# Performance work log

Measured on AMD Instinct MI355X. Metric: run time of the kernel, lower is better.

## Reference

```python
import jax, jax.numpy as jnp
import numpy as np

B, P, C = 4, 2048, 1024
N_HEADS = 16
HEAD = C // N_HEADS


def setup_inputs() -> dict:
    key = jax.random.key(0)
    ks = jax.random.split(key, 9)
    s = C ** -0.5
    return {
        "x": jax.random.normal(ks[0], (B, P, C), dtype=jnp.float32),
        "Wq": jax.random.normal(ks[1], (C, C), dtype=jnp.float32) * s,
        "bq": jnp.zeros((C,), dtype=jnp.float32),
        "Wk": jax.random.normal(ks[2], (C, C), dtype=jnp.float32) * s,
        "bk": jnp.zeros((C,), dtype=jnp.float32),
        "Wv": jax.random.normal(ks[3], (C, C), dtype=jnp.float32) * s,
        "bv": jnp.zeros((C,), dtype=jnp.float32),
        "Wo": jax.random.normal(ks[4], (C, C), dtype=jnp.float32) * s,
        "bo": jnp.zeros((C,), dtype=jnp.float32),
    }


def _attn(x, Wq, bq, Wk, bk, Wv, bv, Wo, bo):
    b, p, c = x.shape
    q = (x @ Wq + bq).reshape(b, p, N_HEADS, HEAD).transpose(0, 2, 1, 3)
    k = (x @ Wk + bk).reshape(b, p, N_HEADS, HEAD).transpose(0, 2, 1, 3)
    v = (x @ Wv + bv).reshape(b, p, N_HEADS, HEAD).transpose(0, 2, 1, 3)
    # scores: [B, H, P, P]
    w = jnp.einsum('bhqd,bhkd->bhqk', q, k) * (HEAD ** -0.5)
    w = jax.nn.softmax(w, axis=-1)
    y = jnp.einsum('bhqk,bhkd->bhqd', w, v)
    y = y.transpose(0, 2, 1, 3).reshape(b, p, c)
    return y @ Wo + bo


def reference(x, Wq, bq, Wk, bk, Wv, bv, Wo, bo):
    return _attn(x, Wq, bq, Wk, bk, Wv, bv, Wo, bo)
```

## Files before the change

kernel.cpp:

```cpp
#include <hip/hip_runtime.h>

#define B_DIM 4
#define P_DIM 2048
#define C_DIM 1024
#define H_CNT 16
#define D_HEAD 64
#define M_DIM 8192
#define K_DIM 1024

typedef __attribute__((ext_vector_type(4))) float  f32x4;
typedef __attribute__((ext_vector_type(8))) __bf16 bf16x8;
typedef __attribute__((ext_vector_type(4))) __bf16 bf16x4;
typedef __attribute__((ext_vector_type(4))) short  s16x4;
typedef __attribute__((ext_vector_type(8))) short  s16x8;

static __device__ __forceinline__ short f2bf(float f) {
    unsigned u = __float_as_uint(f);
    u += 0x7fff + ((u >> 16) & 1);
    return (short)(u >> 16);
}

#define GLDS16(src, dst) __builtin_amdgcn_global_load_lds( \
    (__attribute__((address_space(1))) void*)(void*)(src), \
    (__attribute__((address_space(3))) void*)(void*)(dst), 16, 0, 0)

__global__ __launch_bounds__(256) void cvt_f32_bf16(const float* __restrict__ in,
                                                    short* __restrict__ out) {
    size_t i = ((size_t)blockIdx.x * 256 + threadIdx.x) * 4;
    f32x4 v = *(const f32x4*)(in + i);
    s16x4 o;
    o[0] = f2bf(v[0]); o[1] = f2bf(v[1]); o[2] = f2bf(v[2]); o[3] = f2bf(v[3]);
    *(s16x4*)(out + i) = o;
}

__global__ __launch_bounds__(256) void wtrans_all(const float* __restrict__ W0,
                                                  const float* __restrict__ W1,
                                                  const float* __restrict__ W2,
                                                  const float* __restrict__ W3,
                                                  short* __restrict__ WT) {
    __shared__ float t[32][33];
    const int z = blockIdx.z;
    const float* W = z == 0 ? W0 : z == 1 ? W1 : z == 2 ? W2 : W3;
    short* dst = WT + (size_t)z * C_DIM * C_DIM;
    const int k0 = blockIdx.y * 32, n0 = blockIdx.x * 32;
    const int tx = threadIdx.x & 31, ty = threadIdx.x >> 5;
#pragma unroll
    for (int j = 0; j < 4; ++j)
        t[ty + j * 8][tx] = W[(size_t)(k0 + ty + j * 8) * C_DIM + n0 + tx];
    __syncthreads();
#pragma unroll
    for (int j = 0; j < 4; ++j)
        dst[(size_t)(n0 + ty + j * 8) * C_DIM + k0 + tx] = f2bf(t[tx][ty + j * 8]);
}

__global__ __launch_bounds__(512, 2) void gemm_qk8(const short* __restrict__ A,
                                                   const short* __restrict__ BT,
                                                   const float* __restrict__ bias,
                                                   const float* __restrict__ bias2,
                                                   short* __restrict__ outp) {
    __shared__ __align__(16) short lA[2][256 * 64];
    __shared__ __align__(16) short lB[2][256 * 64];
    const int tid = threadIdx.x;
    const int lane = tid & 63;
    const int w = tid >> 6;
    const int wm = w >> 2, wn = w & 3;
    const int li = lane & 15, g = lane >> 4;

    const int flat = blockIdx.y * 8 + blockIdx.x;
    const int lid = (flat & 7) * 32 + (flat >> 3);
    const int m0 = (lid >> 3) * 256;
    const int n0 = (lid & 7) * 256;

    const int e0 = tid, e1 = tid + 512;
    const int r0 = e0 >> 3, lu0 = (e0 & 7) ^ (r0 & 7);
    const int r1 = e1 >> 3, lu1 = (e1 & 7) ^ (r1 & 7);
    const short* aS0 = A + (size_t)(m0 + r0) * K_DIM + lu0 * 8;
    const short* aS1 = A + (size_t)(m0 + r1) * K_DIM + lu1 * 8;
    const short* bS0 = BT + (size_t)(n0 + r0) * K_DIM + lu0 * 8;
    const short* bS1 = BT + (size_t)(n0 + r1) * K_DIM + lu1 * 8;
    const int dA0 = e0 * 8, dA1 = e1 * 8;

#define STAGE_A8(buf, hh, kt) do { \
    GLDS16(aS0 + (size_t)(hh) * 128 * K_DIM + (kt) * 64, &lA[buf][(hh) * 8192 + dA0]); \
    GLDS16(aS1 + (size_t)(hh) * 128 * K_DIM + (kt) * 64, &lA[buf][(hh) * 8192 + dA1]); } while (0)
#define STAGE_B8(buf, hh, kt) do { \
    GLDS16(bS0 + (size_t)(hh) * 128 * K_DIM + (kt) * 64, &lB[buf][(hh) * 8192 + dB0]); \
    GLDS16(bS1 + (size_t)(hh) * 128 * K_DIM + (kt) * 64, &lB[buf][(hh) * 8192 + dB1]); } while (0)
    const int dB0 = dA0, dB1 = dA1;

    int aoff[8][2], boff[4][2];
#pragma unroll
    for (int mrep = 0; mrep < 8; ++mrep) {
        const int row = wm * 128 + mrep * 16 + li;
#pragma unroll
        for (int ks = 0; ks < 2; ++ks)
            aoff[mrep][ks] = row * 64 + (((ks * 4 + g) ^ (row & 7)) * 8);
    }
#pragma unroll
    for (int nrep = 0; nrep < 4; ++nrep) {
        const int row = wn * 64 + nrep * 16 + li;
#pragma unroll
        for (int ks = 0; ks < 2; ++ks)
            boff[nrep][ks] = row * 64 + (((ks * 4 + g) ^ (row & 7)) * 8);
    }

    f32x4 acc[8][4] = {};

    STAGE_A8(0, 0, 0); STAGE_A8(0, 1, 0);
    STAGE_B8(0, 0, 0); STAGE_B8(0, 1, 0);
    asm volatile("s_waitcnt vmcnt(0)" ::: "memory");
    __builtin_amdgcn_s_barrier();

    for (int t = 0; t < 16; ++t) {
        const int buf = t & 1;
        const short* LA = lA[buf];
        const short* LB = lB[buf];
        bf16x8 bf[4][2];
#pragma unroll
        for (int p = 0; p < 4; ++p) {
            if (p == 0) {
#pragma unroll
                for (int nrep = 0; nrep < 4; ++nrep)
#pragma unroll
                    for (int ks = 0; ks < 2; ++ks)
                        bf[nrep][ks] = *(const bf16x8*)&LB[boff[nrep][ks]];
            }
            bf16x8 af2[2][2];
#pragma unroll
            for (int i = 0; i < 2; ++i)
#pragma unroll
                for (int ks = 0; ks < 2; ++ks)
                    af2[i][ks] = *(const bf16x8*)&LA[aoff[2 * p + i][ks]];
            if (t < 15) {
                if (p == 0)      STAGE_A8(buf ^ 1, 0, t + 1);
                else if (p == 1) STAGE_A8(buf ^ 1, 1, t + 1);
                else if (p == 2) STAGE_B8(buf ^ 1, 0, t + 1);
                else             STAGE_B8(buf ^ 1, 1, t + 1);
            }
            __builtin_amdgcn_s_barrier();
            __builtin_amdgcn_s_setprio(1);
#pragma unroll
            for (int ks = 0; ks < 2; ++ks)
#pragma unroll
                for (int i = 0; i < 2; ++i)
#pragma unroll
                    for (int j = 0; j < 4; ++j)
                        acc[2 * p + i][j] = __builtin_amdgcn_mfma_f32_16x16x32_bf16(
                            bf[j][ks], af2[i][ks], acc[2 * p + i][j], 0, 0, 0);
            __builtin_amdgcn_s_setprio(0);
            __builtin_amdgcn_s_barrier();
        }
        asm volatile("s_waitcnt vmcnt(0)" ::: "memory");
        __builtin_amdgcn_s_barrier();
    }

#pragma unroll
    for (int nrep = 0; nrep < 4; ++nrep) {
        const int nb = n0 + wn * 64 + nrep * 16 + 4 * g;
        const float* bp = nb < 1024 ? bias : bias2;
        const float sc = nb < 1024 ? 0.125f : 1.0f;
        const f32x4 bb = *(const f32x4*)&bp[nb & 1023];
        const int hI = (nb >> 6) & 15, d = nb & 63;
        short* base = outp + (size_t)(nb >> 10) * M_DIM * C_DIM;
#pragma unroll
        for (int mrep = 0; mrep < 8; ++mrep) {
            const int m = m0 + wm * 128 + mrep * 16 + li;
            const int bI = m >> 11, p = m & 2047;
            s16x4 v4;
#pragma unroll
            for (int r = 0; r < 4; ++r) v4[r] = f2bf((acc[mrep][nrep][r] + bb[r]) * sc);
            *(s16x4*)&base[(((size_t)bI * H_CNT + hI) * P_DIM + p) * D_HEAD + d] = v4;
        }
    }
#undef STAGE_A8
#undef STAGE_B8
}

template<int MODE>
__global__ __launch_bounds__(256) void gemm_bt(const short* __restrict__ A,
                                               const short* __restrict__ BT,
                                               const float* __restrict__ bias,
                                               const float* __restrict__ bias2,
                                               void* __restrict__ outp,
                                               int gx) {
    const int h = blockIdx.y * gx + blockIdx.x;
    const int cpx = (gx << 6) >> 3;
    const int lid = (h & 7) * cpx + (h >> 3);
    const int m0 = (lid / gx) * 128;
    const int n0 = (lid % gx) * 128;

    __shared__ __align__(16) short lA[128 * 32];
    __shared__ __align__(16) short lB[128 * 32];
    const int tid = threadIdx.x;
    const int lane = tid & 63;
    const int w = tid >> 6;
    const int wr = (w >> 1) * 64;
    const int wc = (w & 1) * 64;
    const int li = lane & 15, g = lane >> 4;

    f32x4 acc[4][4] = {};

    const int r0s = tid >> 2, r1s = (tid + 256) >> 2;
    const int c0 = (tid & 3) ^ ((r0s >> 1) & 3);
    const int c1 = (tid & 3) ^ ((r1s >> 1) & 3);
    const short* a0 = A + (size_t)(m0 + r0s) * K_DIM + c0 * 8;
    const short* a1 = A + (size_t)(m0 + r1s) * K_DIM + c1 * 8;
    const short* b0 = BT + (size_t)(n0 + r0s) * K_DIM + c0 * 8;
    const short* b1 = BT + (size_t)(n0 + r1s) * K_DIM + c1 * 8;
    short* lA0 = lA + w * 512;  short* lA1 = lA + 2048 + w * 512;
    short* lB0 = lB + w * 512;  short* lB1 = lB + 2048 + w * 512;

    int aoff[4], boff[4];
#pragma unroll
    for (int i = 0; i < 4; ++i) {
        int ra = wr + i * 16 + li;  int pa = g ^ ((ra >> 1) & 3);
        aoff[i] = ra * 32 + pa * 8;
        int rb = wc + i * 16 + li;  int pb = g ^ ((rb >> 1) & 3);
        boff[i] = rb * 32 + pb * 8;
    }

    for (int k0 = 0; k0 < K_DIM; k0 += 32) {
        __syncthreads();
        GLDS16(a0 + k0, lA0);
        GLDS16(a1 + k0, lA1);
        GLDS16(b0 + k0, lB0);
        GLDS16(b1 + k0, lB1);
        __syncthreads();
        bf16x8 af[4], bfr[4];
#pragma unroll
        for (int i = 0; i < 4; ++i) {
            af[i]  = *(const bf16x8*)&lA[aoff[i]];
            bfr[i] = *(const bf16x8*)&lB[boff[i]];
        }
#pragma unroll
        for (int i = 0; i < 4; ++i)
#pragma unroll
            for (int j = 0; j < 4; ++j) {
                if (MODE == 2)
                    acc[i][j] = __builtin_amdgcn_mfma_f32_16x16x32_bf16(
                        af[i], bfr[j], acc[i][j], 0, 0, 0);
                else
                    acc[i][j] = __builtin_amdgcn_mfma_f32_16x16x32_bf16(
                        bfr[j], af[i], acc[i][j], 0, 0, 0);
            }
    }

    if (MODE == 1) {
#pragma unroll
        for (int j = 0; j < 4; ++j) {
            const int nb = n0 + wc + j * 16 + 4 * g;
            const f32x4 bb = *(const f32x4*)&bias[nb];
#pragma unroll
            for (int i = 0; i < 4; ++i) {
                const int m = m0 + wr + i * 16 + li;
                f32x4 v;
#pragma unroll
                for (int r = 0; r < 4; ++r) v[r] = acc[i][j][r] + bb[r];
                *(f32x4*)&((float*)outp)[(size_t)m * C_DIM + nb] = v;
            }
        }
    } else {
#pragma unroll
        for (int j = 0; j < 4; ++j) {
            const int nn = n0 + wc + j * 16 + li;
            const float bb = bias[nn];
            const int hI = nn >> 6, d = nn & 63;
#pragma unroll
            for (int i = 0; i < 4; ++i) {
                const int pbse = m0 + wr + i * 16 + 4 * g;
                const int bI = pbse >> 11, p = pbse & 2047;
                s16x4 v4;
#pragma unroll
                for (int r = 0; r < 4; ++r) v4[r] = f2bf(acc[i][j][r] + bb);
                *(s16x4*)&((short*)outp)[(((size_t)bI * H_CNT + hI) * D_HEAD + d) * P_DIM + p] = v4;
            }
        }
    }
}

__global__ __launch_bounds__(256, 4) void attn_fwd(const short* __restrict__ Q,
                                                   const short* __restrict__ Kb,
                                                   const short* __restrict__ VT,
                                                   short* __restrict__ Y) {
    const int flat = blockIdx.y * 16 + blockIdx.x;
    const int xcd = flat & 7, rr = flat >> 3;
    const int bh = xcd + 8 * (rr >> 4);
    const int qx = rr & 15;

    const int b = bh >> 4, h = bh & 15;
    const int tid = threadIdx.x;
    const int w = tid >> 6, lane = tid & 63;
    const int li = lane & 15, g = lane >> 4;
    const int x7 = li & 7;
    const int q0 = qx * 128 + w * 32;
    const short* Qh = Q + (size_t)bh * P_DIM * D_HEAD;
    const short* Kh = Kb + (size_t)bh * P_DIM * D_HEAD;
    const short* Vh = VT + (size_t)bh * D_HEAD * P_DIM;

    __shared__ __align__(16) short lK[64 * 64];
    __shared__ __align__(16) short lV[64 * 64];
    __shared__ __align__(16) short pb[4][32 * 64];
    short* pw = pb[w];

    bf16x8 qf[2][2];
#pragma unroll
    for (int qt = 0; qt < 2; ++qt)
#pragma unroll
        for (int c = 0; c < 2; ++c)
            qf[qt][c] = *(const bf16x8*)&Qh[(size_t)(q0 + qt * 16 + li) * D_HEAD + c * 32 + g * 8];

    f32x4 o[2][4] = {};
    float ps[2] = {};

    const int t1 = tid + 256;
    const int r0 = tid >> 3, u0 = (tid & 7) ^ (r0 & 7);
    const int r1 = t1 >> 3,  u1 = (t1 & 7) ^ (r1 & 7);
    const short* ks0 = Kh + r0 * D_HEAD + u0 * 8;
    const short* ks1 = Kh + r1 * D_HEAD + u1 * 8;
    const short* vs0 = Vh + r0 * P_DIM + u0 * 8;
    const short* vs1 = Vh + r1 * P_DIM + u1 * 8;
    short* dk0 = lK + tid * 8;  short* dk1 = lK + t1 * 8;
    short* dv0 = lV + tid * 8;  short* dv1 = lV + t1 * 8;

    const int pwrow0 = li * 64;
    const int wsw = x7 << 1;

    for (int k0 = 0; k0 < P_DIM; k0 += 64) {
        __syncthreads();
        GLDS16(ks0 + (size_t)k0 * D_HEAD, dk0);
        GLDS16(ks1 + (size_t)k0 * D_HEAD, dk1);
        GLDS16(vs0 + k0, dv0);
        GLDS16(vs1 + k0, dv1);
        __syncthreads();

        bf16x8 kf[4][2];
#pragma unroll
        for (int kt = 0; kt < 4; ++kt) {
            const int rbase = (kt * 16 + li) * 64;
            kf[kt][0] = *(const bf16x8*)&lK[rbase + ((0 + g) ^ x7) * 8];
            kf[kt][1] = *(const bf16x8*)&lK[rbase + ((4 + g) ^ x7) * 8];
        }

#pragma unroll
        for (int qt = 0; qt < 2; ++qt) {
            f32x4 s[4] = {};
#pragma unroll
            for (int kt = 0; kt < 4; ++kt) {
                s[kt] = __builtin_amdgcn_mfma_f32_16x16x32_bf16(kf[kt][0], qf[qt][0], s[kt], 0, 0, 0);
                s[kt] = __builtin_amdgcn_mfma_f32_16x16x32_bf16(kf[kt][1], qf[qt][1], s[kt], 0, 0, 0);
            }
            const int rowb = pwrow0 + qt * 16 * 64;
#pragma unroll
            for (int kt = 0; kt < 4; ++kt) {
                bf16x4 pv4;
#pragma unroll
                for (int r = 0; r < 4; ++r) {
                    float e = __expf(s[kt][r]);
                    ps[qt] += e;
                    pv4[r] = (__bf16)e;
                }
                const int j = (kt * 4 + g) ^ wsw;
                *(bf16x4*)&pw[rowb + j * 4] = pv4;
            }
        }
        __builtin_amdgcn_sched_barrier(0);
        asm volatile("s_waitcnt lgkmcnt(0)" ::: "memory");
        __builtin_amdgcn_sched_barrier(0);
#pragma unroll
        for (int kc = 0; kc < 2; ++kc) {
            bf16x8 pf[2];
#pragma unroll
            for (int qt = 0; qt < 2; ++qt) {
                const int j = (8 * kc + 2 * g) ^ wsw;
                pf[qt] = *(const bf16x8*)&pw[(qt * 16 + li) * 64 + j * 4];
            }
#pragma unroll
            for (int dt = 0; dt < 4; ++dt) {
                bf16x8 vf = *(const bf16x8*)&lV[(dt * 16 + li) * 64 + ((kc * 4 + g) ^ x7) * 8];
                o[0][dt] = __builtin_amdgcn_mfma_f32_16x16x32_bf16(pf[0], vf, o[0][dt], 0, 0, 0);
                o[1][dt] = __builtin_amdgcn_mfma_f32_16x16x32_bf16(pf[1], vf, o[1][dt], 0, 0, 0);
            }
        }
    }

#pragma unroll
    for (int qt = 0; qt < 2; ++qt) {
        float v = ps[qt];
        v += __shfl_xor(v, 16);
        v += __shfl_xor(v, 32);
#pragma unroll
        for (int r = 0; r < 4; ++r) {
            const float inv = 1.0f / __shfl(v, 4 * g + r);
            const int p = q0 + qt * 16 + 4 * g + r;
            short* yrow = Y + ((size_t)b * P_DIM + p) * C_DIM + h * D_HEAD;
#pragma unroll
            for (int dt = 0; dt < 4; ++dt)
                yrow[dt * 16 + li] = f2bf(o[qt][dt][r] * inv);
        }
    }
}

extern "C" void kernel_launch(void* const* d_in, const int* in_sizes, int n_in,
                              void* d_out, int out_size, void* d_ws, size_t ws_size,
                              hipStream_t stream) {
    (void)in_sizes; (void)n_in; (void)out_size; (void)ws_size;
    const float* x  = (const float*)d_in[0];
    const float* Wq = (const float*)d_in[1];
    const float* bq = (const float*)d_in[2];
    const float* Wk = (const float*)d_in[3];
    const float* bk = (const float*)d_in[4];
    const float* Wv = (const float*)d_in[5];
    const float* bv = (const float*)d_in[6];
    const float* Wo = (const float*)d_in[7];
    const float* bo = (const float*)d_in[8];

    short* ws  = (short*)d_ws;
    short* xb  = ws;
    short* wqt = xb  + (size_t)M_DIM * C_DIM;
    short* wvt = wqt + 2 * (size_t)C_DIM * C_DIM;
    short* wot = wqt + 3 * (size_t)C_DIM * C_DIM;
    short* qd  = wot + (size_t)C_DIM * C_DIM;
    short* kd  = qd  + (size_t)M_DIM * C_DIM;
    short* vtd = kd  + (size_t)M_DIM * C_DIM;
    short* yd  = vtd + (size_t)M_DIM * C_DIM;

    cvt_f32_bf16<<<dim3(M_DIM * C_DIM / 1024), 256, 0, stream>>>(x, xb);
    wtrans_all<<<dim3(32, 32, 4), 256, 0, stream>>>(Wq, Wk, Wv, Wo, wqt);
    gemm_qk8<<<dim3(8, 32), 512, 0, stream>>>(xb, wqt, bq, bk, qd);
    gemm_bt<2><<<dim3(8, 64), 256, 0, stream>>>(xb, wvt, bv, nullptr, (void*)vtd, 8);
    attn_fwd<<<dim3(16, 64), 256, 0, stream>>>(qd, kd, vtd, yd);
    gemm_bt<1><<<dim3(8, 64), 256, 0, stream>>>(yd, wot, bo, nullptr, d_out, 8);
}
```

Before: 194.9 us.

## Replace simple V and output GEMMs with templated 256x128 pipelined 8-wave GEMM

Generalizes the 8-wave, double-buffered, LDS-direct-load QK GEMM into a templated kernel that also runs the V projection (transposed bf16 output) and the output projection (fp32 output) with a 256x128 tile. The old 128x128 single-buffered 4-wave kernels with two syncthreads per k-step are removed. The aim is more reuse per tile and overlap of global loads with MFMA in the two remaining GEMMs. The trade-off is fewer blocks (256 per GEMM) and higher LDS and register use per block.

```diff
diff --git a/kernel.cpp b/kernel.cpp
--- a/kernel.cpp
+++ b/kernel.cpp
@@ -53,13 +53,16 @@
         dst[(size_t)(n0 + ty + j * 8) * C_DIM + k0 + tx] = f2bf(t[tx][ty + j * 8]);
 }
 
-__global__ __launch_bounds__(512, 2) void gemm_qk8(const short* __restrict__ A,
-                                                   const short* __restrict__ BT,
-                                                   const float* __restrict__ bias,
-                                                   const float* __restrict__ bias2,
-                                                   short* __restrict__ outp) {
+template<int MODE>
+__global__ __launch_bounds__(512, 2) void gemm8(const short* __restrict__ A,
+                                                const short* __restrict__ BT,
+                                                const float* __restrict__ bias,
+                                                const float* __restrict__ bias2,
+                                                void* __restrict__ outp) {
+    constexpr int BN = (MODE == 0) ? 256 : 128;
+    constexpr int NREP = BN / 64;
     __shared__ __align__(16) short lA[2][256 * 64];
-    __shared__ __align__(16) short lB[2][256 * 64];
+    __shared__ __align__(16) short lB[2][BN * 64];
     const int tid = threadIdx.x;
     const int lane = tid & 63;
     const int w = tid >> 6;
@@ -69,7 +72,7 @@
     const int flat = blockIdx.y * 8 + blockIdx.x;
     const int lid = (flat & 7) * 32 + (flat >> 3);
     const int m0 = (lid >> 3) * 256;
-    const int n0 = (lid & 7) * 256;
+    const int n0 = (lid & 7) * BN;
 
     const int e0 = tid, e1 = tid + 512;
     const int r0 = e0 >> 3, lu0 = (e0 & 7) ^ (r0 & 7);
@@ -79,6 +82,7 @@
     const short* bS0 = BT + (size_t)(n0 + r0) * K_DIM + lu0 * 8;
     const short* bS1 = BT + (size_t)(n0 + r1) * K_DIM + lu1 * 8;
     const int dA0 = e0 * 8, dA1 = e1 * 8;
+    const int dB0 = dA0, dB1 = dA1;
 
 #define STAGE_A8(buf, hh, kt) do { \
     GLDS16(aS0 + (size_t)(hh) * 128 * K_DIM + (kt) * 64, &lA[buf][(hh) * 8192 + dA0]); \
@@ -86,9 +90,8 @@
 #define STAGE_B8(buf, hh, kt) do { \
     GLDS16(bS0 + (size_t)(hh) * 128 * K_DIM + (kt) * 64, &lB[buf][(hh) * 8192 + dB0]); \
     GLDS16(bS1 + (size_t)(hh) * 128 * K_DIM + (kt) * 64, &lB[buf][(hh) * 8192 + dB1]); } while (0)
-    const int dB0 = dA0, dB1 = dA1;
-
-    int aoff[8][2], boff[4][2];
+
+    int aoff[8][2], boff[NREP][2];
 #pragma unroll
     for (int mrep = 0; mrep < 8; ++mrep) {
         const int row = wm * 128 + mrep * 16 + li;
@@ -97,17 +100,18 @@
             aoff[mrep][ks] = row * 64 + (((ks * 4 + g) ^ (row & 7)) * 8);
     }
 #pragma unroll
-    for (int nrep = 0; nrep < 4; ++nrep) {
-        const int row = wn * 64 + nrep * 16 + li;
+    for (int nrep = 0; nrep < NREP; ++nrep) {
+        const int row = wn * (BN / 4) + nrep * 16 + li;
 #pragma unroll
         for (int ks = 0; ks < 2; ++ks)
             boff[nrep][ks] = row * 64 + (((ks * 4 + g) ^ (row & 7)) * 8);
     }
 
-    f32x4 acc[8][4] = {};
+    f32x4 acc[8][NREP] = {};
 
     STAGE_A8(0, 0, 0); STAGE_A8(0, 1, 0);
-    STAGE_B8(0, 0, 0); STAGE_B8(0, 1, 0);
+    STAGE_B8(0, 0, 0);
+    if (MODE == 0) STAGE_B8(0, 1, 0);
     asm volatile("s_waitcnt vmcnt(0)" ::: "memory");
     __builtin_amdgcn_s_barrier();
 
@@ -115,12 +119,12 @@
         const int buf = t & 1;
         const short* LA = lA[buf];
         const short* LB = lB[buf];
-        bf16x8 bf[4][2];
+        bf16x8 bf[NREP][2];
 #pragma unroll
         for (int p = 0; p < 4; ++p) {
             if (p == 0) {
 #pragma unroll
-                for (int nrep = 0; nrep < 4; ++nrep)
+                for (int nrep = 0; nrep < NREP; ++nrep)
 #pragma unroll
                     for (int ks = 0; ks < 2; ++ks)
                         bf[nrep][ks] = *(const bf16x8*)&LB[boff[nrep][ks]];
@@ -135,7 +139,7 @@
                 if (p == 0)      STAGE_A8(buf ^ 1, 0, t + 1);
                 else if (p == 1) STAGE_A8(buf ^ 1, 1, t + 1);
                 else if (p == 2) STAGE_B8(buf ^ 1, 0, t + 1);
-                else             STAGE_B8(buf ^ 1, 1, t + 1);
+                else if (MODE == 0) STAGE_B8(buf ^ 1, 1, t + 1);
             }
             __builtin_amdgcn_s_barrier();
             __builtin_amdgcn_s_setprio(1);
@@ -144,9 +148,14 @@
 #pragma unroll
                 for (int i = 0; i < 2; ++i)
 #pragma unroll
-                    for (int j = 0; j < 4; ++j)
-                        acc[2 * p + i][j] = __builtin_amdgcn_mfma_f32_16x16x32_bf16(
-                            bf[j][ks], af2[i][ks], acc[2 * p + i][j], 0, 0, 0);
+                    for (int j = 0; j < NREP; ++j) {
+                        if (MODE == 2)
+                            acc[2 * p + i][j] = __builtin_amdgcn_mfma_f32_16x16x32_bf16(
+                                af2[i][ks], bf[j][ks], acc[2 * p + i][j], 0, 0, 0);
+                        else
+                            acc[2 * p + i][j] = __builtin_amdgcn_mfma_f32_16x16x32_bf16(
+                                bf[j][ks], af2[i][ks], acc[2 * p + i][j], 0, 0, 0);
+                    }
             __builtin_amdgcn_s_setprio(0);
             __builtin_amdgcn_s_barrier();
         }
@@ -154,128 +163,58 @@
         __builtin_amdgcn_s_barrier();
     }
 
-#pragma unroll
-    for (int nrep = 0; nrep < 4; ++nrep) {
-        const int nb = n0 + wn * 64 + nrep * 16 + 4 * g;
-        const float* bp = nb < 1024 ? bias : bias2;
-        const float sc = nb < 1024 ? 0.125f : 1.0f;
-        const f32x4 bb = *(const f32x4*)&bp[nb & 1023];
-        const int hI = (nb >> 6) & 15, d = nb & 63;
-        short* base = outp + (size_t)(nb >> 10) * M_DIM * C_DIM;
-#pragma unroll
-        for (int mrep = 0; mrep < 8; ++mrep) {
-            const int m = m0 + wm * 128 + mrep * 16 + li;
-            const int bI = m >> 11, p = m & 2047;
-            s16x4 v4;
-#pragma unroll
-            for (int r = 0; r < 4; ++r) v4[r] = f2bf((acc[mrep][nrep][r] + bb[r]) * sc);
-            *(s16x4*)&base[(((size_t)bI * H_CNT + hI) * P_DIM + p) * D_HEAD + d] = v4;
+    if (MODE == 0) {
+#pragma unroll
+        for (int nrep = 0; nrep < NREP; ++nrep) {
+            const int nb = n0 + wn * 64 + nrep * 16 + 4 * g;
+            const float* bp = nb < 1024 ? bias : bias2;
+            const float sc = nb < 1024 ? 0.125f : 1.0f;
+            const f32x4 bb = *(const f32x4*)&bp[nb & 1023];
+            const int hI = (nb >> 6) & 15, d = nb & 63;
+            short* base = (short*)outp + (size_t)(nb >> 10) * M_DIM * C_DIM;
+#pragma unroll
+            for (int mrep = 0; mrep < 8; ++mrep) {
+                const int m = m0 + wm * 128 + mrep * 16 + li;
+                const int bI = m >> 11, p = m & 2047;
+                s16x4 v4;
+#pragma unroll
+                for (int r = 0; r < 4; ++r) v4[r] = f2bf((acc[mrep][nrep][r] + bb[r]) * sc);
+                *(s16x4*)&base[(((size_t)bI * H_CNT + hI) * P_DIM + p) * D_HEAD + d] = v4;
+            }
+        }
+    } else if (MODE == 1) {
+#pragma unroll
+        for (int nrep = 0; nrep < NREP; ++nrep) {
+            const int nb = n0 + wn * 32 + nrep * 16 + 4 * g;
+            const f32x4 bb = *(const f32x4*)&bias[nb];
+#pragma unroll
+            for (int mrep = 0; mrep < 8; ++mrep) {
+                const int m = m0 + wm * 128 + mrep * 16 + li;
+                f32x4 v;
+#pragma unroll
+                for (int r = 0; r < 4; ++r) v[r] = acc[mrep][nrep][r] + bb[r];
+                *(f32x4*)&((float*)outp)[(size_t)m * C_DIM + nb] = v;
+            }
+        }
+    } else {
+#pragma unroll
+        for (int nrep = 0; nrep < NREP; ++nrep) {
+            const int n = n0 + wn * 32 + nrep * 16 + li;
+            const float bb = bias[n];
+            const int hI = n >> 6, d = n & 63;
+#pragma unroll
+            for (int mrep = 0; mrep < 8; ++mrep) {
+                const int pbse = m0 + wm * 128 + mrep * 16 + 4 * g;
+                const int bI = pbse >> 11, p = pbse & 2047;
+                s16x4 v4;
+#pragma unroll
+                for (int r = 0; r < 4; ++r) v4[r] = f2bf(acc[mrep][nrep][r] + bb);
+                *(s16x4*)&((short*)outp)[(((size_t)bI * H_CNT + hI) * D_HEAD + d) * P_DIM + p] = v4;
+            }
         }
     }
 #undef STAGE_A8
 #undef STAGE_B8
-}
-
-template<int MODE>
-__global__ __launch_bounds__(256) void gemm_bt(const short* __restrict__ A,
-                                               const short* __restrict__ BT,
-                                               const float* __restrict__ bias,
-                                               const float* __restrict__ bias2,
-                                               void* __restrict__ outp,
-                                               int gx) {
-    const int h = blockIdx.y * gx + blockIdx.x;
-    const int cpx = (gx << 6) >> 3;
-    const int lid = (h & 7) * cpx + (h >> 3);
-    const int m0 = (lid / gx) * 128;
-    const int n0 = (lid % gx) * 128;
-
-    __shared__ __align__(16) short lA[128 * 32];
-    __shared__ __align__(16) short lB[128 * 32];
-    const int tid = threadIdx.x;
-    const int lane = tid & 63;
-    const int w = tid >> 6;
-    const int wr = (w >> 1) * 64;
-    const int wc = (w & 1) * 64;
-    const int li = lane & 15, g = lane >> 4;
-
-    f32x4 acc[4][4] = {};
-
-    const int r0s = tid >> 2, r1s = (tid + 256) >> 2;
-    const int c0 = (tid & 3) ^ ((r0s >> 1) & 3);
-    const int c1 = (tid & 3) ^ ((r1s >> 1) & 3);
-    const short* a0 = A + (size_t)(m0 + r0s) * K_DIM + c0 * 8;
-    const short* a1 = A + (size_t)(m0 + r1s) * K_DIM + c1 * 8;
-    const short* b0 = BT + (size_t)(n0 + r0s) * K_DIM + c0 * 8;
-    const short* b1 = BT + (size_t)(n0 + r1s) * K_DIM + c1 * 8;
-    short* lA0 = lA + w * 512;  short* lA1 = lA + 2048 + w * 512;
-    short* lB0 = lB + w * 512;  short* lB1 = lB + 2048 + w * 512;
-
-    int aoff[4], boff[4];
-#pragma unroll
-    for (int i = 0; i < 4; ++i) {
-        int ra = wr + i * 16 + li;  int pa = g ^ ((ra >> 1) & 3);
-        aoff[i] = ra * 32 + pa * 8;
-        int rb = wc + i * 16 + li;  int pb = g ^ ((rb >> 1) & 3);
-        boff[i] = rb * 32 + pb * 8;
-    }
-
-    for (int k0 = 0; k0 < K_DIM; k0 += 32) {
-        __syncthreads();
-        GLDS16(a0 + k0, lA0);
-        GLDS16(a1 + k0, lA1);
-        GLDS16(b0 + k0, lB0);
-        GLDS16(b1 + k0, lB1);
-        __syncthreads();
-        bf16x8 af[4], bfr[4];
-#pragma unroll
-        for (int i = 0; i < 4; ++i) {
-            af[i]  = *(const bf16x8*)&lA[aoff[i]];
-            bfr[i] = *(const bf16x8*)&lB[boff[i]];
-        }
-#pragma unroll
-        for (int i = 0; i < 4; ++i)
-#pragma unroll
-            for (int j = 0; j < 4; ++j) {
-                if (MODE == 2)
-                    acc[i][j] = __builtin_amdgcn_mfma_f32_16x16x32_bf16(
-                        af[i], bfr[j], acc[i][j], 0, 0, 0);
-                else
-                    acc[i][j] = __builtin_amdgcn_mfma_f32_16x16x32_bf16(
-                        bfr[j], af[i], acc[i][j], 0, 0, 0);
-            }
-    }
-
-    if (MODE == 1) {
-#pragma unroll
-        for (int j = 0; j < 4; ++j) {
-            const int nb = n0 + wc + j * 16 + 4 * g;
-            const f32x4 bb = *(const f32x4*)&bias[nb];
-#pragma unroll
-            for (int i = 0; i < 4; ++i) {
-                const int m = m0 + wr + i * 16 + li;
-                f32x4 v;
-#pragma unroll
-                for (int r = 0; r < 4; ++r) v[r] = acc[i][j][r] + bb[r];
-                *(f32x4*)&((float*)outp)[(size_t)m * C_DIM + nb] = v;
-            }
-        }
-    } else {
-#pragma unroll
-        for (int j = 0; j < 4; ++j) {
-            const int nn = n0 + wc + j * 16 + li;
-            const float bb = bias[nn];
-            const int hI = nn >> 6, d = nn & 63;
-#pragma unroll
-            for (int i = 0; i < 4; ++i) {
-                const int pbse = m0 + wr + i * 16 + 4 * g;
-                const int bI = pbse >> 11, p = pbse & 2047;
-                s16x4 v4;
-#pragma unroll
-                for (int r = 0; r < 4; ++r) v4[r] = f2bf(acc[i][j][r] + bb);
-                *(s16x4*)&((short*)outp)[(((size_t)bI * H_CNT + hI) * D_HEAD + d) * P_DIM + p] = v4;
-            }
-        }
-    }
 }
 
 __global__ __launch_bounds__(256, 4) void attn_fwd(const short* __restrict__ Q,
@@ -426,8 +365,8 @@
 
     cvt_f32_bf16<<<dim3(M_DIM * C_DIM / 1024), 256, 0, stream>>>(x, xb);
     wtrans_all<<<dim3(32, 32, 4), 256, 0, stream>>>(Wq, Wk, Wv, Wo, wqt);
-    gemm_qk8<<<dim3(8, 32), 512, 0, stream>>>(xb, wqt, bq, bk, qd);
-    gemm_bt<2><<<dim3(8, 64), 256, 0, stream>>>(xb, wvt, bv, nullptr, (void*)vtd, 8);
+    gemm8<0><<<dim3(8, 32), 512, 0, stream>>>(xb, wqt, bq, bk, qd);
+    gemm8<2><<<dim3(8, 32), 512, 0, stream>>>(xb, wvt, bv, nullptr, vtd);
     attn_fwd<<<dim3(16, 64), 256, 0, stream>>>(qd, kd, vtd, yd);
-    gemm_bt<1><<<dim3(8, 64), 256, 0, stream>>>(yd, wot, bo, nullptr, d_out, 8);
-}
+    gemm8<1><<<dim3(8, 32), 512, 0, stream>>>(yd, wot, bo, nullptr, d_out);
+}
```

Measured after the change: 200.6 us. 1.03x slower.
